# Kernel tuning notes

Measured on AMD Instinct MI355X. Metric: run time of the kernel, lower is better.

## Reference

```python
import jax, jax.numpy as jnp
import numpy as np

NUM_EXPERTS = 4

def setup_inputs() -> dict:
    key = jax.random.key(0)
    k = jax.random.split(key, 6)
    B, S, D = 8, 4096, 1024
    H = D * 2  # mlp_ratio = 2
    x = jax.random.normal(k[0], (B, S, D), dtype=jnp.float32)
    expert_mask = jax.random.randint(k[1], (B, S), 0, NUM_EXPERTS, dtype=jnp.int32)
    w1 = jax.random.normal(k[2], (H, D), dtype=jnp.float32) * (D ** -0.5)
    b1 = jax.random.normal(k[3], (H,), dtype=jnp.float32) * 0.02
    w2 = jax.random.normal(k[4], (D, H), dtype=jnp.float32) * (H ** -0.5)
    b2 = jax.random.normal(k[5], (D,), dtype=jnp.float32) * 0.02
    return {"x": x, "expert_mask": expert_mask, "w1": w1, "b1": b1, "w2": w2, "b2": b2}


def reference(x, expert_mask, w1, b1, w2, b2):
    """Nested SwiGLU MLP with token-wise expert-dependent active hidden width.

    Expert e in [0, E) activates the first Hh * 2^(e+1-E) units of each of the
    gate/up branches (Hh = H/2); the largest expert (e = E-1) uses the full width.
    out = (silu(gate) * up masked to active width) @ W2[:, :Hh].T + b2
    """
    E = NUM_EXPERTS
    H = w1.shape[0]
    Hh = H // 2  # per-branch (gate / up) width
    # dense expand: z = x @ W1.T + b1  -> [B, S, H]
    z = jnp.einsum('bsd,hd->bsh', x, w1) + b1
    g = z[..., :Hh]  # gate branch
    u = z[..., Hh:]  # up branch
    # active width per token: Hh // 2^(E-1-e)
    active = Hh // (2 ** (E - 1 - expert_mask))  # [B, S] int
    mask = (jnp.arange(Hh) < active[..., None]).astype(x.dtype)  # [B, S, Hh]
    a = jax.nn.silu(g) * u * mask  # zeros outside the token's nested width
    out = jnp.einsum('bsh,dh->bsd', a, w2[:, :Hh]) + b2
    return out
```

## Files before the change

kernel.cpp:

```cpp
#include <hip/hip_runtime.h>
#include <stdint.h>


typedef __attribute__((ext_vector_type(8))) __bf16 bf16x8;
typedef __attribute__((ext_vector_type(4))) float f32x4;

#define MFMA16(a, b, c) __builtin_amdgcn_mfma_f32_16x16x32_bf16(a, b, c, 0, 0, 0)

#define BAR() asm volatile("s_barrier" ::: "memory")
#define VMCNT(n) asm volatile("s_waitcnt vmcnt(" #n ")" ::: "memory")

static __device__ __forceinline__ unsigned short f2bf(float f) {
  union { float f; uint32_t u; } v; v.f = f;
  uint32_t r = v.u + 0x7FFFu + ((v.u >> 16) & 1u);
  return (unsigned short)(r >> 16);
}

static __device__ __forceinline__ void gload_lds16(const void* g, void* l) {
  __builtin_amdgcn_global_load_lds(
      (const __attribute__((address_space(1))) void*)g,
      (__attribute__((address_space(3))) void*)l, 16, 0, 0);
}

__global__ void conv_w_kernel(const float* __restrict__ w1,
                              const float* __restrict__ w2,
                              unsigned short* __restrict__ w1b,
                              unsigned short* __restrict__ w2b) {
  int bid = blockIdx.x;
  if (bid < 2048) {
    int i = bid * 256 + threadIdx.x;
    float4 v = ((const float4*)w1)[i];
    ushort4 o; o.x = f2bf(v.x); o.y = f2bf(v.y); o.z = f2bf(v.z); o.w = f2bf(v.w);
    ((ushort4*)w1b)[i] = o;
  } else {
    int i = (bid - 2048) * 256 + threadIdx.x;
    int d = i >> 8;
    int h4 = (i & 255) * 4;
    float4 v = *(const float4*)(w2 + (size_t)d * 2048 + h4);
    ushort4 o; o.x = f2bf(v.x); o.y = f2bf(v.y); o.z = f2bf(v.z); o.w = f2bf(v.w);
    *(ushort4*)(w2b + (size_t)d * 1024 + h4) = o;
  }
}

__global__ void hist_kernel(const int* __restrict__ emask, int* __restrict__ hist) {
  __shared__ int h[4];
  int tid = threadIdx.x;
  if (tid < 4) h[tid] = 0;
  __syncthreads();
  int e = emask[blockIdx.x * 128 + tid];
  atomicAdd(&h[e], 1);
  __syncthreads();
  if (tid < 4) hist[blockIdx.x * 4 + tid] = h[tid];
}

__global__ void scan_kernel(const int* __restrict__ hist, int* __restrict__ off) {
  __shared__ int total[4];
  int tid = threadIdx.x;
  if (tid < 4) {
    int s = 0;
    for (int b = 0; b < 256; ++b) s += hist[b * 4 + tid];
    total[tid] = s;
  }
  __syncthreads();
  if (tid < 4) {
    int base = 0;
    for (int j = 0; j < tid; ++j) base += total[j];
    int run = base;
    for (int b = 0; b < 256; ++b) {
      off[b * 4 + tid] = run;
      run += hist[b * 4 + tid];
    }
  }
}

__global__ void scatter_kernel(const int* __restrict__ emask,
                               const int* __restrict__ off,
                               int* __restrict__ perm, int* __restrict__ em_sorted) {
  __shared__ int c0[4];
  int tid = threadIdx.x;
  int lane = tid & 63, wid = tid >> 6;
  int t = blockIdx.x * 128 + tid;
  int e = emask[t];
  unsigned long long b0 = __ballot(e == 0);
  unsigned long long b1 = __ballot(e == 1);
  unsigned long long b2 = __ballot(e == 2);
  unsigned long long b3 = __ballot(e == 3);
  if (tid == 0) {
    c0[0] = __popcll(b0); c0[1] = __popcll(b1);
    c0[2] = __popcll(b2); c0[3] = __popcll(b3);
  }
  __syncthreads();
  unsigned long long mine = (e == 0) ? b0 : (e == 1) ? b1 : (e == 2) ? b2 : b3;
  int rank = __popcll(mine & ((1ull << lane) - 1ull));
  if (wid) rank += c0[e];
  int pos = off[blockIdx.x * 4 + e] + rank;
  perm[pos] = t;
  em_sorted[pos] = e;
}

__global__ void xconv_kernel(const float* __restrict__ x, const int* __restrict__ perm,
                             unsigned short* __restrict__ xs) {
  int gid = blockIdx.x * 256 + threadIdx.x;
  int s = gid >> 7;
  int seg = gid & 127;
  int tok = perm[s];
  const float* src = x + (size_t)tok * 1024 + seg * 8;
  float4 v0 = *(const float4*)(src);
  float4 v1 = *(const float4*)(src + 4);
  bf16x8 hv;
  hv[0] = (__bf16)v0.x; hv[1] = (__bf16)v0.y; hv[2] = (__bf16)v0.z; hv[3] = (__bf16)v0.w;
  hv[4] = (__bf16)v1.x; hv[5] = (__bf16)v1.y; hv[6] = (__bf16)v1.z; hv[7] = (__bf16)v1.w;
  *(bf16x8*)(xs + (size_t)s * 1024 + seg * 8) = hv;
}

static __device__ __forceinline__ int block_max_e(const int* em_sorted, int m0,
                                                  int tid, int* sred) {
  int v = 0;
  if (tid < 128) v = em_sorted[m0 + tid];
  #pragma unroll
  for (int o = 32; o; o >>= 1) v = max(v, __shfl_xor(v, o));
  if ((tid & 63) == 0) sred[tid >> 6] = v;
  __syncthreads();
  return max(sred[0], sred[1]);
}

__global__ __launch_bounds__(256, 4)
void gemm1_sorted_kernel(const unsigned short* __restrict__ xs,
                         const int* __restrict__ em_sorted,
                         const unsigned short* __restrict__ w1b,
                         const float* __restrict__ b1,
                         unsigned short* __restrict__ a_out) {
  __shared__ __align__(16) char lds[32768];
  __shared__ int sred[4];
  char* AS = lds;
  char* BS = lds + 16384;

  const int tid = threadIdx.x;
  const int lane = tid & 63;
  const int w = tid >> 6;
  const int wm = w & 1;
  const int wn = w >> 1;
  const int m0 = blockIdx.x * 128;
  const int n0 = blockIdx.y * 64;

  int maxe = block_max_e(em_sorted, m0, tid, sred);
  if (n0 >= (128 << maxe)) return;

  f32x4 accg[4][2] = {};
  f32x4 accu[4][2] = {};

  for (int k0 = 0; k0 < 1024; k0 += 64) {
    #pragma unroll
    for (int i = 0; i < 4; ++i) {
      int c = (w * 4 + i) * 64 + lane;
      int p = c * 16;
      int r = p >> 7;
      int kb16 = ((p >> 4) & 7) ^ (r & 7);
      gload_lds16((const char*)xs + (((size_t)(m0 + r) * 1024 + k0) * 2) + kb16 * 16,
                  AS + (w * 4 + i) * 1024);
      int h = (r < 64) ? (n0 + r) : (1024 + n0 + (r - 64));
      gload_lds16((const char*)w1b + (((size_t)h * 1024 + k0) * 2) + kb16 * 16,
                  BS + (w * 4 + i) * 1024);
    }
    __syncthreads();
    #pragma unroll
    for (int kk = 0; kk < 2; ++kk) {
      const int kbyte = kk * 64 + (lane >> 4) * 16;
      bf16x8 af[4], bg[2], bu[2];
      #pragma unroll
      for (int m = 0; m < 4; ++m) {
        int r = wm * 64 + m * 16 + (lane & 15);
        int o = (r * 128 + kbyte) ^ ((r & 7) << 4);
        af[m] = *(const bf16x8*)(AS + o);
      }
      #pragma unroll
      for (int n = 0; n < 2; ++n) {
        int r = wn * 32 + n * 16 + (lane & 15);
        int o = (r * 128 + kbyte) ^ ((r & 7) << 4);
        bg[n] = *(const bf16x8*)(BS + o);
        bu[n] = *(const bf16x8*)(BS + 8192 + o);
      }
      #pragma unroll
      for (int m = 0; m < 4; ++m)
        #pragma unroll
        for (int n = 0; n < 2; ++n) {
          accg[m][n] = MFMA16(af[m], bg[n], accg[m][n]);
          accu[m][n] = MFMA16(af[m], bu[n], accu[m][n]);
        }
    }
    __syncthreads();
  }
  #pragma unroll
  for (int m = 0; m < 4; ++m) {
    int rbase = m0 + wm * 64 + m * 16 + (lane >> 4) * 4;
    int act[4];
    #pragma unroll
    for (int r = 0; r < 4; ++r) act[r] = 128 << em_sorted[rbase + r];
    #pragma unroll
    for (int n = 0; n < 2; ++n) {
      int col = n0 + wn * 32 + n * 16 + (lane & 15);
      float b1g = b1[col], b1u = b1[col + 1024];
      #pragma unroll
      for (int r = 0; r < 4; ++r) {
        float g = accg[m][n][r] + b1g;
        float u = accu[m][n][r] + b1u;
        float s = g / (1.f + __expf(-g));
        float val = (col < act[r]) ? (s * u) : 0.f;
        a_out[(size_t)(rbase + r) * 1024 + col] = f2bf(val);
      }
    }
  }
}

static __device__ __forceinline__ void ds_loadA(const char* Abase, int lane,
                                                bf16x8 (&af)[4][2], int mh) {
  #pragma unroll
  for (int mf = 0; mf < 4; ++mf)
    #pragma unroll
    for (int kk = 0; kk < 2; ++kk) {
      int r = mh * 64 + mf * 16 + (lane & 15);
      int o = (r * 128 + kk * 64 + ((lane >> 4) * 16)) ^ ((r & 7) << 4);
      af[mf][kk] = *(const bf16x8*)(Abase + o);
    }
}

static __device__ __forceinline__ void ds_loadB(const char* Bbase, int lane, int wc,
                                                bf16x8 (&bf)[2][2], int nh) {
  #pragma unroll
  for (int nl = 0; nl < 2; ++nl)
    #pragma unroll
    for (int kk = 0; kk < 2; ++kk) {
      int n = nh * 2 + nl;
      int r = (wc & 1) * 64 + n * 16 + (lane & 15);
      int o = (r * 128 + kk * 64 + ((lane >> 4) * 16)) ^ ((r & 7) << 4);
      bf[nl][kk] = *(const bf16x8*)(Bbase + o);
    }
}

static __device__ __forceinline__ void mfma_quad(bf16x8 (&af)[4][2], bf16x8 (&bf)[2][2],
                                                 f32x4 (&acc)[8][4], int mh, int nh) {
  __builtin_amdgcn_s_setprio(1);
  #pragma unroll
  for (int mf = 0; mf < 4; ++mf)
    #pragma unroll
    for (int nl = 0; nl < 2; ++nl)
      #pragma unroll
      for (int kk = 0; kk < 2; ++kk)
        acc[mh * 4 + mf][nh * 2 + nl] =
            MFMA16(af[mf][kk], bf[nl][kk], acc[mh * 4 + mf][nh * 2 + nl]);
  __builtin_amdgcn_s_setprio(0);
}

template <class ST>
static __device__ __forceinline__ void kpair_steady(const ST& st, char* lds, int j,
    int lane, int wr, int wc, bf16x8 (&af)[4][2], bf16x8 (&bf0)[2][2],
    bf16x8 (&bf1)[2][2], f32x4 (&acc)[8][4]) {
  const int a = 2 * j, b = 2 * j + 1;
  const char* Aa = lds + (a & 1) * 32768 + wr * 16384;
  const char* Ab = lds + (b & 1) * 32768 + wr * 16384;
  const char* Ba = lds + 65536 + (a & 1) * 32768 + (wc >> 1) * 16384;
  const char* Bb = lds + 65536 + (b & 1) * 32768 + (wc >> 1) * 16384;
  ds_loadA(Aa, lane, af, 0); ds_loadB(Ba, lane, wc, bf0, 0);
  st.stageA(b, 0);            BAR(); mfma_quad(af, bf0, acc, 0, 0); BAR();
  ds_loadB(Ba, lane, wc, bf1, 1);
  st.stageA(b, 1);            BAR(); mfma_quad(af, bf1, acc, 0, 1); BAR();
  ds_loadA(Aa, lane, af, 1);
  st.stageB(a + 2, 0);        BAR(); mfma_quad(af, bf0, acc, 1, 0); BAR();
  st.stageB(a + 2, 1); VMCNT(4); BAR(); mfma_quad(af, bf1, acc, 1, 1); BAR();
  ds_loadA(Ab, lane, af, 0); ds_loadB(Bb, lane, wc, bf0, 0);
  st.stageA(a + 2, 0);        BAR(); mfma_quad(af, bf0, acc, 0, 0); BAR();
  ds_loadB(Bb, lane, wc, bf1, 1);
  st.stageA(a + 2, 1);        BAR(); mfma_quad(af, bf1, acc, 0, 1); BAR();
  ds_loadA(Ab, lane, af, 1);
  st.stageB(b + 2, 0);        BAR(); mfma_quad(af, bf0, acc, 1, 0); BAR();
  st.stageB(b + 2, 1); VMCNT(4); BAR(); mfma_quad(af, bf1, acc, 1, 1); BAR();
}

template <class ST>
static __device__ __forceinline__ void kpair_last(const ST& st, char* lds, int j,
    int lane, int wr, int wc, bf16x8 (&af)[4][2], bf16x8 (&bf0)[2][2],
    bf16x8 (&bf1)[2][2], f32x4 (&acc)[8][4]) {
  const int a = 2 * j, b = 2 * j + 1;
  const char* Aa = lds + (a & 1) * 32768 + wr * 16384;
  const char* Ab = lds + (b & 1) * 32768 + wr * 16384;
  const char* Ba = lds + 65536 + (a & 1) * 32768 + (wc >> 1) * 16384;
  const char* Bb = lds + 65536 + (b & 1) * 32768 + (wc >> 1) * 16384;
  ds_loadA(Aa, lane, af, 0); ds_loadB(Ba, lane, wc, bf0, 0);
  st.stageA(b, 0); BAR(); mfma_quad(af, bf0, acc, 0, 0); BAR();
  ds_loadB(Ba, lane, wc, bf1, 1);
  st.stageA(b, 1); BAR(); mfma_quad(af, bf1, acc, 0, 1); BAR();
  ds_loadA(Aa, lane, af, 1);
  BAR(); mfma_quad(af, bf0, acc, 1, 0); BAR();
  VMCNT(0); BAR(); mfma_quad(af, bf1, acc, 1, 1); BAR();
  ds_loadA(Ab, lane, af, 0); ds_loadB(Bb, lane, wc, bf0, 0);
  BAR(); mfma_quad(af, bf0, acc, 0, 0); BAR();
  ds_loadB(Bb, lane, wc, bf1, 1);
  BAR(); mfma_quad(af, bf1, acc, 0, 1); BAR();
  ds_loadA(Ab, lane, af, 1);
  BAR(); mfma_quad(af, bf0, acc, 1, 0); BAR();
  mfma_quad(af, bf1, acc, 1, 1);
}

template <class ST>
static __device__ __forceinline__ void prologue(const ST& st) {
  st.stageA(0, 0); st.stageA(0, 1);
  st.stageB(0, 0); st.stageB(0, 1);
  st.stageB(1, 0); st.stageB(1, 1);
  VMCNT(4); BAR();
}

#define STAGE_DECODE(kb)                         \
  int r = (kb) * 8 + (lane >> 3);                \
  int s = (lane & 7) ^ (r & 7);

struct G2Stage {
  const char* a_in; const char* w2b; char* lds; int m0, n0; int w, lane;
  __device__ __forceinline__ void stageA(int t, int half) const {
    char* dst = lds + (t & 1) * 32768 + half * 16384;
    #pragma unroll
    for (int i = 0; i < 2; ++i) {
      int kb = w * 2 + i;
      STAGE_DECODE(kb)
      gload_lds16(a_in + (size_t)(m0 + half * 128 + r) * 2048 + t * 128 + s * 16,
                  dst + kb * 1024);
    }
  }
  __device__ __forceinline__ void stageB(int t, int half) const {
    char* dst = lds + 65536 + (t & 1) * 32768 + half * 16384;
    #pragma unroll
    for (int i = 0; i < 2; ++i) {
      int kb = w * 2 + i;
      STAGE_DECODE(kb)
      gload_lds16(w2b + (size_t)(n0 + half * 128 + r) * 2048 + t * 128 + s * 16,
                  dst + kb * 1024);
    }
  }
};

__global__ __launch_bounds__(512, 2)
void gemm2_kernel8(const unsigned short* __restrict__ a_in,
                   const int* __restrict__ em_sorted,
                   const int* __restrict__ perm,
                   const unsigned short* __restrict__ w2b,
                   const float* __restrict__ b2, float* __restrict__ out) {
  __shared__ __align__(16) char lds[131072];
  const int tid = threadIdx.x, lane = tid & 63, w = tid >> 6;
  const int wr = w >> 2, wc = w & 3;
  const int m0 = (127 - blockIdx.y) * 256, n0 = blockIdx.x * 256;

  int v = em_sorted[m0 + (tid & 255)];
  #pragma unroll
  for (int o = 32; o; o >>= 1) v = max(v, __shfl_xor(v, o));
  int* sred = (int*)lds;
  if (lane == 0) sred[w] = v;
  __syncthreads();
  int maxe = sred[0];
  #pragma unroll
  for (int i = 1; i < 8; ++i) maxe = max(maxe, sred[i]);
  __syncthreads();
  const int J = 1 << maxe;

  G2Stage st{(const char*)a_in, (const char*)w2b, lds, m0, n0, w, lane};
  f32x4 acc[8][4] = {};
  bf16x8 af[4][2], bf0[2][2], bf1[2][2];

  prologue(st);
  #pragma clang loop unroll(disable)
  for (int j = 0; j < J - 1; ++j)
    kpair_steady(st, lds, j, lane, wr, wc, af, bf0, bf1, acc);
  kpair_last(st, lds, J - 1, lane, wr, wc, af, bf0, bf1, acc);

  #pragma unroll
  for (int p = 0; p < 2; ++p) {
    __syncthreads();
    if (wr == p) {
      #pragma unroll
      for (int mf = 0; mf < 8; ++mf)
        #pragma unroll
        for (int nf = 0; nf < 4; ++nf) {
          int col = wc * 64 + nf * 16 + (lane & 15);
          #pragma unroll
          for (int rr = 0; rr < 4; ++rr) {
            int rl = mf * 16 + (lane >> 4) * 4 + rr;
            int byte = (rl * 1024 + col * 4) ^ (((rl >> 2) & 3) << 6);
            *(float*)(lds + byte) = acc[mf][nf][rr];
          }
        }
    }
    __syncthreads();
    float4 bb = *(const float4*)(b2 + n0 + lane * 4);
    #pragma unroll
    for (int i = 0; i < 16; ++i) {
      int rl = i * 8 + w;
      int tok = perm[m0 + p * 128 + rl];
      int byte = (rl * 1024 + lane * 16) ^ (((rl >> 2) & 3) << 6);
      float4 vv = *(const float4*)(lds + byte);
      vv.x += bb.x; vv.y += bb.y; vv.z += bb.z; vv.w += bb.w;
      *(float4*)(out + (size_t)tok * 1024 + n0 + lane * 4) = vv;
    }
  }
}

extern "C" void kernel_launch(void* const* d_in, const int* in_sizes, int n_in,
                              void* d_out, int out_size, void* d_ws, size_t ws_size,
                              hipStream_t stream) {
  const float* x  = (const float*)d_in[0];
  const int* em   = (const int*)d_in[1];
  const float* w1 = (const float*)d_in[2];
  const float* b1 = (const float*)d_in[3];
  const float* w2 = (const float*)d_in[4];
  const float* b2 = (const float*)d_in[5];
  float* out = (float*)d_out;

  char* ws = (char*)d_ws;
  unsigned short* a_ws = (unsigned short*)ws;
  unsigned short* w1b  = (unsigned short*)(ws + 67108864);
  unsigned short* w2b  = (unsigned short*)(ws + 71303168);
  unsigned short* xs   = (unsigned short*)(ws + 73400320);
  int* perm      = (int*)(ws + 140509184);
  int* em_sorted = (int*)(ws + 140640256);
  int* hist      = (int*)(ws + 140771328);
  int* off       = (int*)(ws + 140775424);

  conv_w_kernel<<<3072, 256, 0, stream>>>(w1, w2, w1b, w2b);
  hist_kernel<<<256, 128, 0, stream>>>(em, hist);
  scan_kernel<<<1, 64, 0, stream>>>(hist, off);
  scatter_kernel<<<256, 128, 0, stream>>>(em, off, perm, em_sorted);
  xconv_kernel<<<16384, 256, 0, stream>>>(x, perm, xs);
  gemm1_sorted_kernel<<<dim3(256, 16), 256, 0, stream>>>(xs, em_sorted, w1b, b1, a_ws);
  gemm2_kernel8<<<dim3(4, 128), 512, 0, stream>>>(a_ws, em_sorted, perm, w2b, b2, out);
}
```

Before: 200.2 us.

## Fuse x gather and bf16 conversion into gemm1 A-tile load

Removes the separate xconv kernel that gathered token rows by permutation and wrote a bf16 copy of x. Gemm1 now reads fp32 x directly through perm, converts it to bf16 in registers and stores it into swizzled LDS, which saves a full write and reread of the 64 MB staging buffer. The cost is that x is reloaded and reconverted once per N-tile block (up to 16 times) and the A load becomes synchronous register traffic instead of async global-to-LDS. Block order along M is also reversed so the wide-expert tiles are scheduled first.

After: 210.1 us. 4.9% more time.

```diff
diff --git a/kernel.cpp b/kernel.cpp
--- a/kernel.cpp
+++ b/kernel.cpp
@@ -98,21 +98,6 @@
   em_sorted[pos] = e;
 }
 
-__global__ void xconv_kernel(const float* __restrict__ x, const int* __restrict__ perm,
-                             unsigned short* __restrict__ xs) {
-  int gid = blockIdx.x * 256 + threadIdx.x;
-  int s = gid >> 7;
-  int seg = gid & 127;
-  int tok = perm[s];
-  const float* src = x + (size_t)tok * 1024 + seg * 8;
-  float4 v0 = *(const float4*)(src);
-  float4 v1 = *(const float4*)(src + 4);
-  bf16x8 hv;
-  hv[0] = (__bf16)v0.x; hv[1] = (__bf16)v0.y; hv[2] = (__bf16)v0.z; hv[3] = (__bf16)v0.w;
-  hv[4] = (__bf16)v1.x; hv[5] = (__bf16)v1.y; hv[6] = (__bf16)v1.z; hv[7] = (__bf16)v1.w;
-  *(bf16x8*)(xs + (size_t)s * 1024 + seg * 8) = hv;
-}
-
 static __device__ __forceinline__ int block_max_e(const int* em_sorted, int m0,
                                                   int tid, int* sred) {
   int v = 0;
@@ -125,7 +110,8 @@
 }
 
 __global__ __launch_bounds__(256, 4)
-void gemm1_sorted_kernel(const unsigned short* __restrict__ xs,
+void gemm1_sorted_kernel(const float* __restrict__ x,
+                         const int* __restrict__ perm,
                          const int* __restrict__ em_sorted,
                          const unsigned short* __restrict__ w1b,
                          const float* __restrict__ b1,
@@ -140,11 +126,17 @@
   const int w = tid >> 6;
   const int wm = w & 1;
   const int wn = w >> 1;
-  const int m0 = blockIdx.x * 128;
+  const int m0 = (255 - blockIdx.x) * 128;
   const int n0 = blockIdx.y * 64;
 
   int maxe = block_max_e(em_sorted, m0, tid, sred);
   if (n0 >= (128 << maxe)) return;
+
+  const int arow = tid >> 3;
+  const int aseg = tid & 7;
+  int toks[4];
+  #pragma unroll
+  for (int it = 0; it < 4; ++it) toks[it] = perm[m0 + arow + it * 32];
 
   f32x4 accg[4][2] = {};
   f32x4 accu[4][2] = {};
@@ -156,11 +148,23 @@
       int p = c * 16;
       int r = p >> 7;
       int kb16 = ((p >> 4) & 7) ^ (r & 7);
-      gload_lds16((const char*)xs + (((size_t)(m0 + r) * 1024 + k0) * 2) + kb16 * 16,
-                  AS + (w * 4 + i) * 1024);
       int h = (r < 64) ? (n0 + r) : (1024 + n0 + (r - 64));
       gload_lds16((const char*)w1b + (((size_t)h * 1024 + k0) * 2) + kb16 * 16,
                   BS + (w * 4 + i) * 1024);
+    }
+    #pragma unroll
+    for (int it = 0; it < 4; ++it) {
+      int row = arow + it * 32;
+      const float* src = x + (size_t)toks[it] * 1024 + k0 + aseg * 8;
+      float4 v0 = *(const float4*)(src);
+      float4 v1 = *(const float4*)(src + 4);
+      bf16x8 hv;
+      hv[0] = (__bf16)v0.x; hv[1] = (__bf16)v0.y;
+      hv[2] = (__bf16)v0.z; hv[3] = (__bf16)v0.w;
+      hv[4] = (__bf16)v1.x; hv[5] = (__bf16)v1.y;
+      hv[6] = (__bf16)v1.z; hv[7] = (__bf16)v1.w;
+      int o = (row * 128 + aseg * 16) ^ ((row & 7) << 4);
+      *(bf16x8*)(AS + o) = hv;
     }
     __syncthreads();
     #pragma unroll
@@ -416,7 +420,6 @@
   unsigned short* a_ws = (unsigned short*)ws;
   unsigned short* w1b  = (unsigned short*)(ws + 67108864);
   unsigned short* w2b  = (unsigned short*)(ws + 71303168);
-  unsigned short* xs   = (unsigned short*)(ws + 73400320);
   int* perm      = (int*)(ws + 140509184);
   int* em_sorted = (int*)(ws + 140640256);
   int* hist      = (int*)(ws + 140771328);
@@ -426,7 +429,6 @@
   hist_kernel<<<256, 128, 0, stream>>>(em, hist);
   scan_kernel<<<1, 64, 0, stream>>>(hist, off);
   scatter_kernel<<<256, 128, 0, stream>>>(em, off, perm, em_sorted);
-  xconv_kernel<<<16384, 256, 0, stream>>>(x, perm, xs);
-  gemm1_sorted_kernel<<<dim3(256, 16), 256, 0, stream>>>(xs, em_sorted, w1b, b1, a_ws);
+  gemm1_sorted_kernel<<<dim3(256, 16), 256, 0, stream>>>(x, perm, em_sorted, w1b, b1, a_ws);
   gemm2_kernel8<<<dim3(4, 128), 512, 0, stream>>>(a_ws, em_sorted, perm, w2b, b2, out);
 }
```
